# Performance work log

Measured on AMD Instinct MI355X. Metric: run time of the kernel, lower is better.

Reference implementation:

```python
import jax, jax.numpy as jnp
import numpy as np

N = 50000      # nodes
E = 800000     # edges (avg degree 16)
D_IN = 128
D_H = 128
D_OUT = 64
SLOPE = 0.2    # leaky-relu negative slope (from the 0.2 constants in the graph)


def setup_inputs() -> dict:
    key = jax.random.key(0)
    ks = jax.random.split(key, 18)
    def w(k, shape, fan_in):
        return jax.random.normal(k, shape, jnp.float32) / np.sqrt(fan_in)
    inp = {
        "x": jax.random.normal(ks[0], (N, D_IN), jnp.float32),
        "W0": w(ks[1], (D_IN, D_H), D_IN),
        "b0": jnp.zeros((D_H,), jnp.float32),
        "Wq1": w(ks[2], (D_H, D_H), D_H),
        "bq1": jnp.zeros((D_H,), jnp.float32),
        "Wp1": w(ks[3], (D_H, D_H), D_H),
        "bp1": jnp.zeros((D_H,), jnp.float32),
        "a1": 0.1 * w(ks[4], (D_H,), D_H),
        "bg2": jnp.zeros((D_H,), jnp.float32),
        "Wq2": w(ks[5], (D_H, D_OUT), D_H),
        "bq2": jnp.zeros((D_OUT,), jnp.float32),
        "Wp2": w(ks[6], (D_H, D_OUT), D_H),
        "bp2": jnp.zeros((D_OUT,), jnp.float32),
        "a2": 0.1 * w(ks[7], (D_OUT,), D_OUT),
        "b_out": jnp.zeros((D_OUT,), jnp.float32),
        "src": jax.random.randint(ks[8], (E,), 0, N),
        "dst": jax.random.randint(ks[9], (E,), 0, N),
        "num_nodes": N,
    }
    return inp


def _gat_block(m, src, dst, Wq, bq, Wp, bp, a, n):
    # m: [N, d_in]; q/p: [N, d]
    q = m @ Wq + bq
    p = m @ Wp + bp
    # edge scores: s_e = sum_d leaky_relu(q[dst_e] + p[src_e]) * a_d   [E]
    e = jax.nn.leaky_relu(q[dst] + p[src], SLOPE)          # [E, d]
    s = jnp.einsum("ed,d->e", e, a)                        # [E]
    es = jnp.exp(s)                                        # unstabilized exp, as in source graph
    denom = jax.ops.segment_sum(es, dst, num_segments=n)   # [N]
    alpha = es / denom[dst]                                # [E] edge softmax over incoming edges
    # aggregate messages alpha_e * p[src_e] into dst nodes
    agg = jax.ops.segment_sum(alpha[:, None] * p[src], dst, num_segments=n)  # [N, d]
    return agg


def reference(x, W0, b0, Wq1, bq1, Wp1, bp1, a1, bg2, Wq2, bq2, Wp2, bp2, a2, b_out, src, dst, num_nodes):
    m1 = jax.nn.gelu(x @ W0 + b0, approximate=False)       # erf GELU per graph constants
    h1 = _gat_block(m1, src, dst, Wq1, bq1, Wp1, bp1, a1, num_nodes)
    m2 = jax.nn.gelu(h1 + bg2, approximate=False)
    h2 = _gat_block(m2, src, dst, Wq2, bq2, Wp2, bp2, a2, num_nodes)
    return h2 + b_out
```

## Files before the change

kernel.cpp:

```cpp
#include <hip/hip_runtime.h>
#include <hip/hip_bf16.h>
#include <math.h>


#define SLOPE 0.2f

typedef __attribute__((ext_vector_type(8))) __bf16 bf16x8;
typedef __attribute__((ext_vector_type(4))) float f32x4;

__device__ __forceinline__ float gelu_erf(float x) {
    return 0.5f * x * (1.0f + erff(x * 0.70710678118654752f));
}

__device__ __forceinline__ unsigned short f2bf(float f) {
    unsigned int u = __float_as_uint(f);
    return (unsigned short)((u + 0x7fffu + ((u >> 16) & 1u)) >> 16);
}
__device__ __forceinline__ float bf2f(unsigned short h) {
    return __uint_as_float((unsigned int)h << 16);
}

__device__ __forceinline__ float row16_sum(float x) {
    x += __int_as_float(__builtin_amdgcn_update_dpp(0, __float_as_int(x), 0x121, 0xF, 0xF, true));
    x += __int_as_float(__builtin_amdgcn_update_dpp(0, __float_as_int(x), 0x122, 0xF, 0xF, true));
    x += __int_as_float(__builtin_amdgcn_update_dpp(0, __float_as_int(x), 0x124, 0xF, 0xF, true));
    x += __int_as_float(__builtin_amdgcn_update_dpp(0, __float_as_int(x), 0x128, 0xF, 0xF, true));
    return x;
}

__device__ __forceinline__ int swz(int off) { return off ^ ((off >> 4) & 0x70); }

__global__ __launch_bounds__(256) void pack_w(
    const float* __restrict__ W0,  const float* __restrict__ Wq1,
    const float* __restrict__ Wp1, const float* __restrict__ Wq2,
    const float* __restrict__ Wp2,
    unsigned short* __restrict__ P0,  unsigned short* __restrict__ Pq1,
    unsigned short* __restrict__ Pp1, unsigned short* __restrict__ Pq2,
    unsigned short* __restrict__ Pp2)
{
    const float* W; unsigned short* P; int C;
    switch (blockIdx.y) {
        case 0:  W = W0;  P = P0;  C = 128; break;
        case 1:  W = Wq1; P = Pq1; C = 128; break;
        case 2:  W = Wp1; P = Pp1; C = 128; break;
        case 3:  W = Wq2; P = Pq2; C = 64;  break;
        default: W = Wp2; P = Pp2; C = 64;  break;
    }
    int i = blockIdx.x * 256 + threadIdx.x;
    int CE = C * 128;
    if (i >= CE) return;
    int j = i & 7, l = (i >> 3) & 63, ks = (i >> 9) & 3, ct = i >> 11;
    int k = ks * 32 + ((l >> 4) << 3) + j;
    int n = ct * 16 + (l & 15);
    float v = W[k * C + n];
    unsigned short hb = f2bf(v);
    P[i] = hb;
    P[CE + i] = f2bf(v - bf2f(hb));
}

template <int C, bool TWO, int EPI>
__global__ __launch_bounds__(256) void mfma_gemm(
    const float* __restrict__ Af,
    const unsigned short* __restrict__ AHg, const unsigned short* __restrict__ ALg,
    const unsigned short* __restrict__ P1, const float* __restrict__ b1,
    const unsigned short* __restrict__ P2, const float* __restrict__ b2,
    float* __restrict__ outq, unsigned short* __restrict__ outp,
    unsigned short* __restrict__ o1hi, unsigned short* __restrict__ o1lo,
    int N)
{
    constexpr int CE  = C * 128;
    constexpr int CTT = (TWO ? 2 : 1) * (C / 16);
    constexpr int CTW = CTT / 4;
    constexpr int QCT = C / 16;

    __shared__ __align__(16) unsigned char lds[32768];

    const int t = threadIdx.x;
    const int lane = t & 63;
    const int w = t >> 6;
    const int row0 = blockIdx.x * 64;
    const int mcol = lane & 15;
    const int hk = lane >> 4;

    if constexpr (EPI == 0) {
#pragma unroll
        for (int i = 0; i < 8; i++) {
            int idx = t + i * 256;
            int row = idx >> 5;
            int gr = row0 + row;
            float4 v = make_float4(0.f, 0.f, 0.f, 0.f);
            if (gr < N) v = *reinterpret_cast<const float4*>(Af + (size_t)gr * 128 + (idx & 31) * 4);
            const float* f = reinterpret_cast<const float*>(&v);
            unsigned int h[4], l[4];
#pragma unroll
            for (int j = 0; j < 4; j++) {
                unsigned short hb = f2bf(f[j]);
                h[j] = hb;
                l[j] = f2bf(f[j] - bf2f(hb));
            }
            int so = swz(row * 256 + (idx & 31) * 8);
            *reinterpret_cast<uint2*>(&lds[so])         = make_uint2(h[0] | (h[1] << 16), h[2] | (h[3] << 16));
            *reinterpret_cast<uint2*>(&lds[16384 + so]) = make_uint2(l[0] | (l[1] << 16), l[2] | (l[3] << 16));
        }
    } else {
#pragma unroll
        for (int i = 0; i < 4; i++) {
            int idx = t + i * 256;
            int row = idx >> 4;
            int gr = row0 + row;
            uint4 vh = make_uint4(0, 0, 0, 0), vl = make_uint4(0, 0, 0, 0);
            if (gr < N) {
                vh = *reinterpret_cast<const uint4*>(AHg + (size_t)gr * 128 + (idx & 15) * 8);
                vl = *reinterpret_cast<const uint4*>(ALg + (size_t)gr * 128 + (idx & 15) * 8);
            }
            int so = swz(row * 256 + (idx & 15) * 16);
            *reinterpret_cast<uint4*>(&lds[so])         = vh;
            *reinterpret_cast<uint4*>(&lds[16384 + so]) = vl;
        }
    }
    __syncthreads();

    f32x4 acc[CTW][4];
#pragma unroll
    for (int c = 0; c < CTW; c++)
#pragma unroll
        for (int rf = 0; rf < 4; rf++) acc[c][rf] = (f32x4){0.f, 0.f, 0.f, 0.f};

#pragma unroll
    for (int ks = 0; ks < 4; ks++) {
        bf16x8 ah[4], al[4];
#pragma unroll
        for (int rf = 0; rf < 4; rf++) {
            int so = swz((rf * 16 + mcol) * 256 + ks * 64 + hk * 16);
            ah[rf] = *reinterpret_cast<const bf16x8*>(&lds[so]);
            al[rf] = *reinterpret_cast<const bf16x8*>(&lds[16384 + so]);
        }
#pragma unroll
        for (int c = 0; c < CTW; c++) {
            int ctg = w * CTW + c;
            bool isq = (!TWO) || (ctg < QCT);
            int ct = isq ? ctg : ctg - QCT;
            const unsigned short* P = isq ? P1 : P2;
            const unsigned short* Wp = P + ((ct * 4 + ks) * 64 + lane) * 8;
            bf16x8 bh = *reinterpret_cast<const bf16x8*>(Wp);
            bf16x8 bl = *reinterpret_cast<const bf16x8*>(Wp + CE);
#pragma unroll
            for (int rf = 0; rf < 4; rf++) {
                acc[c][rf] = __builtin_amdgcn_mfma_f32_16x16x32_bf16(ah[rf], bh, acc[c][rf], 0, 0, 0);
                acc[c][rf] = __builtin_amdgcn_mfma_f32_16x16x32_bf16(al[rf], bh, acc[c][rf], 0, 0, 0);
                acc[c][rf] = __builtin_amdgcn_mfma_f32_16x16x32_bf16(ah[rf], bl, acc[c][rf], 0, 0, 0);
            }
        }
    }

    __syncthreads();

    if constexpr (EPI == 0) {
#pragma unroll
        for (int c = 0; c < CTW; c++) {
            int col = (w * CTW + c) * 16 + mcol;
            float bv = b1[col];
#pragma unroll
            for (int rf = 0; rf < 4; rf++) {
#pragma unroll
                for (int r = 0; r < 4; r++) {
                    int row = rf * 16 + hk * 4 + r;
                    float v = gelu_erf(acc[c][rf][r] + bv);
                    unsigned short hb = f2bf(v);
                    int bo = row * 256 + col * 2;
                    *reinterpret_cast<unsigned short*>(&lds[swz(bo)])         = hb;
                    *reinterpret_cast<unsigned short*>(&lds[16384 + swz(bo)]) = f2bf(v - bf2f(hb));
                }
            }
        }
        __syncthreads();
#pragma unroll
        for (int i = 0; i < 8; i++) {
            int idx = t + i * 256;
            int pl = idx >> 10;
            int j = idx & 1023;
            int row = j >> 4;
            int gr = row0 + row;
            if (gr < N) {
                uint4 v = *reinterpret_cast<const uint4*>(&lds[pl * 16384 + swz(row * 256 + (j & 15) * 16)]);
                unsigned short* dp = pl ? o1lo : o1hi;
                *reinterpret_cast<uint4*>(dp + (size_t)gr * 128 + (j & 15) * 8) = v;
            }
        }
    } else {
#pragma unroll
        for (int c = 0; c < CTW; c++) {
            int ctg = w * CTW + c;
            bool isq = ctg < QCT;
            int ct = isq ? ctg : ctg - QCT;
            int col = ct * 16 + mcol;
            float bv = (isq ? b1 : b2)[col];
#pragma unroll
            for (int rf = 0; rf < 4; rf++) {
#pragma unroll
                for (int r = 0; r < 4; r++) {
                    int row = rf * 16 + hk * 4 + r;
                    int gr = row0 + row;
                    float v = acc[c][rf][r] + bv;
                    if (isq) {
                        if (gr < N) outq[(size_t)gr * C + col] = v;
                    } else {
                        *reinterpret_cast<unsigned short*>(&lds[swz(row * 256 + col * 2)]) = f2bf(v);
                    }
                }
            }
        }
        __syncthreads();
        constexpr int SLOTS = C / 8;
#pragma unroll
        for (int i = 0; i < (64 * SLOTS) / 256; i++) {
            int idx = t + i * 256;
            int row = idx / SLOTS;
            int sl = idx % SLOTS;
            int gr = row0 + row;
            if (gr < N)
                *reinterpret_cast<uint4*>(outp + (size_t)gr * C + sl * 8) =
                    *reinterpret_cast<const uint4*>(&lds[swz(row * 256 + sl * 16)]);
        }
    }
}


__global__ __launch_bounds__(256) void hist_coarse(
    const int* __restrict__ dst, int* __restrict__ gh, int E, int CB)
{
    __shared__ int cnt[4096];
    const int blk = blockIdx.x;
    const int t = threadIdx.x;
    for (int b = t; b < CB; b += 256) cnt[b] = 0;
    __syncthreads();
    const int epb = (E + 63) / 64;
    const int s = blk * epb;
    const int e_ = (s + epb < E) ? s + epb : E;
    for (int i = s + t; i < e_; i += 256)
        atomicAdd(&cnt[dst[i] >> 4], 1);
    __syncthreads();
    for (int b = t; b < CB; b += 256)
        gh[b * 64 + blk] = cnt[b];
}

__global__ __launch_bounds__(256) void scan1_kernel(const int* __restrict__ gh,
                                                    int* __restrict__ gscan,
                                                    int* __restrict__ bsum, int M)
{
    __shared__ int lds[256];
    int t = threadIdx.x;
    int i = blockIdx.x * 256 + t;
    int v = (i < M) ? gh[i] : 0;
    lds[t] = v;
    __syncthreads();
    int x = v;
    for (int off = 1; off < 256; off <<= 1) {
        int y = (t >= off) ? lds[t - off] : 0;
        __syncthreads();
        x += y;
        lds[t] = x;
        __syncthreads();
    }
    if (i < M) gscan[i] = x - v;
    if (t == 255) bsum[blockIdx.x] = x;
}

__global__ __launch_bounds__(1024) void scan2_kernel(int* __restrict__ bsum, int NB)
{
    __shared__ int lds[1024];
    int t = threadIdx.x;
    int v = (t < NB) ? bsum[t] : 0;
    lds[t] = v;
    __syncthreads();
    int x = v;
    for (int off = 1; off < 1024; off <<= 1) {
        int y = (t >= off) ? lds[t - off] : 0;
        __syncthreads();
        x += y;
        lds[t] = x;
        __syncthreads();
    }
    if (t < NB) bsum[t] = x - v;
}

__global__ __launch_bounds__(256) void scan3_kernel(int* __restrict__ gscan,
                                                    const int* __restrict__ bsum, int M)
{
    int i = blockIdx.x * 256 + threadIdx.x;
    if (i < M) gscan[i] += bsum[blockIdx.x];
}

__global__ __launch_bounds__(256) void scatter_coarse(
    const int* __restrict__ src, const int* __restrict__ dst,
    const int* __restrict__ gscan, int2* __restrict__ pairs, int E, int CB)
{
    __shared__ int cur[4096];
    const int blk = blockIdx.x;
    const int t = threadIdx.x;
    for (int b = t; b < CB; b += 256)
        cur[b] = gscan[b * 64 + blk];
    __syncthreads();
    const int epb = (E + 63) / 64;
    const int s = blk * epb;
    const int e_ = (s + epb < E) ? s + epb : E;
    for (int i = s + t; i < e_; i += 256) {
        int d = dst[i];
        int sv = src[i];
        int pos = atomicAdd(&cur[d >> 4], 1);
        pairs[pos] = make_int2(d, sv);
    }
}

__global__ __launch_bounds__(256) void finalize_kernel(
    const int2* __restrict__ pairs, const int* __restrict__ gscan,
    int* __restrict__ offs, int* __restrict__ csr_src, int N, int E, int CB)
{
    const int wid = blockIdx.x * 4 + (threadIdx.x >> 6);
    const int lane = threadIdx.x & 63;
    if (wid >= CB) return;

    const int s    = gscan[wid * 64];
    const int e_   = (wid + 1 < CB) ? gscan[(wid + 1) * 64] : E;
    const int base = wid * 16;
    const unsigned long long ltmask = (lane == 63) ? ~0ull >> 1
                                                   : (1ull << lane) - 1ull;

    int rc[16];
#pragma unroll
    for (int j = 0; j < 16; j++) rc[j] = 0;
    for (int c0 = s; c0 < e_; c0 += 64) {
        int i = c0 + lane;
        int d = (i < e_) ? pairs[i].x - base : -1;
#pragma unroll
        for (int j = 0; j < 16; j++)
            rc[j] += (int)__popcll(__ballot(d == j));
    }

    int pref[16];
    int run = s;
#pragma unroll
    for (int j = 0; j < 16; j++) { pref[j] = run; run += rc[j]; }
    int pref_v = 0;
#pragma unroll
    for (int j = 0; j < 16; j++) pref_v = (lane == j) ? pref[j] : pref_v;

    if (lane < 16 && base + lane < N) offs[base + lane] = pref_v;
    if (wid == CB - 1 && lane == 16) offs[N] = E;

    int rcv = 0;
    for (int c0 = s; c0 < e_; c0 += 64) {
        int i = c0 + lane;
        const bool act = i < e_;
        int2 pr = act ? pairs[i] : make_int2(base - 1, 0);
        int d = pr.x - base;
        unsigned long long msel = 0;
        int addcnt = 0;
#pragma unroll
        for (int j = 0; j < 16; j++) {
            unsigned long long m = __ballot(d == j);
            if (d == j) msel = m;
            if (lane == j) addcnt = (int)__popcll(m);
        }
        int subrank = (int)__popcll(msel & ltmask);
        int posbase = __builtin_amdgcn_ds_bpermute(d * 4, pref_v + rcv);
        if (act) csr_src[posbase + subrank] = pr.y;
        rcv += addcnt;
    }
}

template <int D, int EPI>
__global__ __launch_bounds__(256) void gat_agg(
    const float* __restrict__ q, const unsigned short* __restrict__ p,
    const float* __restrict__ a, const float* __restrict__ bvec,
    const int* __restrict__ offs, const int* __restrict__ csr_src,
    float* __restrict__ out, unsigned short* __restrict__ mhi,
    unsigned short* __restrict__ mlo, int N)
{
    constexpr int VPL = D / 16;
    const int t = threadIdx.x;
    const int lane = t & 63;
    const int sl = lane & 15;
    const int base = sl * VPL;
    const int node = blockIdx.x * 16 + ((t >> 6) << 2) + (lane >> 4);
    const bool valid = node < N;

    float qv[VPL], a6[VPL], a4[VPL], acc[VPL];
#pragma unroll
    for (int v = 0; v < VPL; v++) { qv[v] = 0.f; acc[v] = 0.f; }
    if (valid) {
        const float* qp = q + (size_t)node * D + base;
        float4 q0 = *reinterpret_cast<const float4*>(qp);
        qv[0] = q0.x; qv[1] = q0.y; qv[2] = q0.z; qv[3] = q0.w;
        if constexpr (VPL == 8) {
            float4 q1 = *reinterpret_cast<const float4*>(qp + 4);
            qv[4] = q1.x; qv[5] = q1.y; qv[6] = q1.z; qv[7] = q1.w;
        }
    }
#pragma unroll
    for (int v = 0; v < VPL; v++) {
        float av = a[base + v];
        a6[v] = 0.6f * av;
        a4[v] = 0.4f * av;
    }

    auto gather = [&](int s) -> uint4 {
        if constexpr (D == 128) {
            return *reinterpret_cast<const uint4*>(p + (size_t)s * 128 + base);
        } else {
            uint2 u = *reinterpret_cast<const uint2*>(p + (size_t)s * 64 + base);
            return make_uint4(u.x, u.y, 0u, 0u);
        }
    };
    auto unpack = [&](uint4 u, float* pv) {
        pv[0] = __uint_as_float(u.x << 16); pv[1] = __uint_as_float(u.x & 0xffff0000u);
        pv[2] = __uint_as_float(u.y << 16); pv[3] = __uint_as_float(u.y & 0xffff0000u);
        if constexpr (VPL == 8) {
            pv[4] = __uint_as_float(u.z << 16); pv[5] = __uint_as_float(u.z & 0xffff0000u);
            pv[6] = __uint_as_float(u.w << 16); pv[7] = __uint_as_float(u.w & 0xffff0000u);
        }
    };

    float denom = 0.f;
    int e  = valid ? offs[node] : 0;
    int e1 = valid ? offs[node + 1] : 0;

    int s0 = csr_src[(e + 0 < e1) ? e + 0 : 0];
    int s1 = csr_src[(e + 1 < e1) ? e + 1 : 0];
    int s2 = csr_src[(e + 2 < e1) ? e + 2 : 0];
    int s3 = csr_src[(e + 3 < e1) ? e + 3 : 0];
    uint4 uA0 = gather(s0), uA1 = gather(s1), uA2 = gather(s2), uA3 = gather(s3);
    int en = e + 4;
    int n0 = csr_src[(en + 0 < e1) ? en + 0 : 0];
    int n1 = csr_src[(en + 1 < e1) ? en + 1 : 0];
    int n2 = csr_src[(en + 2 < e1) ? en + 2 : 0];
    int n3 = csr_src[(en + 3 < e1) ? en + 3 : 0];

    while (__any(e < e1)) {
        const bool a0 = (e + 0) < e1, a1b = (e + 1) < e1,
                   a2 = (e + 2) < e1, a3 = (e + 3) < e1;

        uint4 v0 = gather(n0), v1 = gather(n1), v2 = gather(n2), v3 = gather(n3);

        const int em = en + 4;
        const int m0 = csr_src[(em + 0 < e1) ? em + 0 : 0];
        const int m1 = csr_src[(em + 1 < e1) ? em + 1 : 0];
        const int m2 = csr_src[(em + 2 < e1) ? em + 2 : 0];
        const int m3 = csr_src[(em + 3 < e1) ? em + 3 : 0];

        float pv[4][VPL];
        unpack(uA0, pv[0]); unpack(uA1, pv[1]); unpack(uA2, pv[2]); unpack(uA3, pv[3]);

        float pa0 = 0.f, pa1 = 0.f, pa2 = 0.f, pa3 = 0.f;
#pragma unroll
        for (int v = 0; v < VPL; v++) {
            float d0 = qv[v] + pv[0][v];
            float d1 = qv[v] + pv[1][v];
            float d2 = qv[v] + pv[2][v];
            float d3 = qv[v] + pv[3][v];
            pa0 = fmaf(d0, a6[v], pa0); pa0 = fmaf(fabsf(d0), a4[v], pa0);
            pa1 = fmaf(d1, a6[v], pa1); pa1 = fmaf(fabsf(d1), a4[v], pa1);
            pa2 = fmaf(d2, a6[v], pa2); pa2 = fmaf(fabsf(d2), a4[v], pa2);
            pa3 = fmaf(d3, a6[v], pa3); pa3 = fmaf(fabsf(d3), a4[v], pa3);
        }

        float r0 = row16_sum(pa0);
        float r1 = row16_sum(pa1);
        float r2 = row16_sum(pa2);
        float r3 = row16_sum(pa3);

        float esm0 = a0  ? __expf(r0) : 0.f;
        float esm1 = a1b ? __expf(r1) : 0.f;
        float esm2 = a2  ? __expf(r2) : 0.f;
        float esm3 = a3  ? __expf(r3) : 0.f;
        denom += (esm0 + esm1) + (esm2 + esm3);
#pragma unroll
        for (int v = 0; v < VPL; v++) {
            acc[v] = fmaf(esm0, pv[0][v], acc[v]);
            acc[v] = fmaf(esm1, pv[1][v], acc[v]);
            acc[v] = fmaf(esm2, pv[2][v], acc[v]);
            acc[v] = fmaf(esm3, pv[3][v], acc[v]);
        }

        uA0 = v0; uA1 = v1; uA2 = v2; uA3 = v3;
        n0 = m0; n1 = m1; n2 = m2; n3 = m3;
        e = en; en = em;
    }

    if (!valid) return;
    float inv = (denom != 0.f) ? 1.f / denom : 0.f;
    if constexpr (EPI == 0) {
        union { unsigned short us[8]; uint4 v; } H, L;
#pragma unroll
        for (int v = 0; v < VPL; v++) {
            float g = gelu_erf(acc[v] * inv + bvec[base + v]);
            H.us[v] = f2bf(g);
            L.us[v] = f2bf(g - bf2f(H.us[v]));
        }
        *reinterpret_cast<uint4*>(mhi + (size_t)node * 128 + base) = H.v;
        *reinterpret_cast<uint4*>(mlo + (size_t)node * 128 + base) = L.v;
    } else {
        union { float f[4]; float4 v; } O;
#pragma unroll
        for (int v = 0; v < VPL; v++) O.f[v] = acc[v] * inv + bvec[base + v];
        *reinterpret_cast<float4*>(out + (size_t)node * D + base) = O.v;
    }
}

extern "C" void kernel_launch(void* const* d_in, const int* in_sizes, int n_in,
                              void* d_out, int out_size, void* d_ws, size_t ws_size,
                              hipStream_t stream)
{
    const float* x     = (const float*)d_in[0];
    const float* W0    = (const float*)d_in[1];
    const float* b0    = (const float*)d_in[2];
    const float* Wq1   = (const float*)d_in[3];
    const float* bq1   = (const float*)d_in[4];
    const float* Wp1   = (const float*)d_in[5];
    const float* bp1   = (const float*)d_in[6];
    const float* a1    = (const float*)d_in[7];
    const float* bg2   = (const float*)d_in[8];
    const float* Wq2   = (const float*)d_in[9];
    const float* bq2   = (const float*)d_in[10];
    const float* Wp2   = (const float*)d_in[11];
    const float* bp2   = (const float*)d_in[12];
    const float* a2    = (const float*)d_in[13];
    const float* b_out = (const float*)d_in[14];
    const int*   src   = (const int*)d_in[15];
    const int*   dst   = (const int*)d_in[16];

    const int N = in_sizes[0] / 128;
    const int E = in_sizes[15];
    float* out = (float*)d_out;

    float* q_buf        = (float*)d_ws;
    unsigned short* pb  = (unsigned short*)(q_buf + (size_t)N * 128);
    unsigned short* Mhi = pb + (size_t)N * 128;
    unsigned short* Mlo = Mhi + (size_t)N * 128;
    unsigned short* P0  = Mlo + (size_t)N * 128;
    unsigned short* Pq1 = P0  + 128 * 128 * 2;
    unsigned short* Pp1 = Pq1 + 128 * 128 * 2;
    unsigned short* Pq2 = Pp1 + 128 * 128 * 2;
    unsigned short* Pp2 = Pq2 + 128 * 64 * 2;
    int* offs    = (int*)(Pp2 + 128 * 64 * 2);
    int* csr_src = offs + (N + 2);
    const int CB = (N + 15) / 16;
    const int M  = CB * 64;
    int* gh    = csr_src + E;
    int* gscan = gh + M;
    int* bsum  = gscan + M;
    int2* pairs = (int2*)q_buf;

    const int NB1 = (M + 255) / 256;

    pack_w<<<dim3(64, 5), 256, 0, stream>>>(W0, Wq1, Wp1, Wq2, Wp2,
                                            P0, Pq1, Pp1, Pq2, Pp2);
    hist_coarse<<<64, 256, 0, stream>>>(dst, gh, E, CB);
    scan1_kernel<<<NB1, 256, 0, stream>>>(gh, gscan, bsum, M);
    scan2_kernel<<<1, 1024, 0, stream>>>(bsum, NB1);
    scan3_kernel<<<NB1, 256, 0, stream>>>(gscan, bsum, M);
    scatter_coarse<<<64, 256, 0, stream>>>(src, dst, gscan, pairs, E, CB);
    finalize_kernel<<<(CB + 3) / 4, 256, 0, stream>>>(pairs, gscan, offs, csr_src, N, E, CB);

    const int GB64 = (N + 63) / 64;
    const int GGAT = (N + 15) / 16;

    mfma_gemm<128, false, 0><<<GB64, 256, 0, stream>>>(
        x, nullptr, nullptr, P0, b0, nullptr, nullptr,
        nullptr, nullptr, Mhi, Mlo, N);
    mfma_gemm<128, true, 1><<<GB64, 256, 0, stream>>>(
        nullptr, Mhi, Mlo, Pq1, bq1, Pp1, bp1,
        q_buf, pb, nullptr, nullptr, N);
    gat_agg<128, 0><<<GGAT, 256, 0, stream>>>(
        q_buf, pb, a1, bg2, offs, csr_src,
        nullptr, Mhi, Mlo, N);
    mfma_gemm<64, true, 1><<<GB64, 256, 0, stream>>>(
        nullptr, Mhi, Mlo, Pq2, bq2, Pp2, bp2,
        q_buf, pb, nullptr, nullptr, N);
    gat_agg<64, 1><<<GGAT, 256, 0, stream>>>(
        q_buf, pb, a2, b_out, offs, csr_src,
        out, nullptr, nullptr, N);
}
```

Before: 283.6 us.

## Fuse input GEMM with layer-1 q/p projection GEMM via LDS

Merges the first GEMM (x@W0 + GELU) and the layer-1 q/p projection GEMM into one kernel. The GELU output stays in LDS as a bf16 hi/lo split and is fed directly into the second GEMM, so the Mhi/Mlo intermediates are no longer written to and read back from global memory, and one launch goes away. The template GEMM is also specialised into a separate 64-column kernel for layer 2. The cost is a heavier kernel with more accumulator registers, which may reduce occupancy.

```diff
diff --git a/kernel.cpp b/kernel.cpp
--- a/kernel.cpp
+++ b/kernel.cpp
@@ -58,21 +58,14 @@
     P[CE + i] = f2bf(v - bf2f(hb));
 }
 
-template <int C, bool TWO, int EPI>
-__global__ __launch_bounds__(256) void mfma_gemm(
-    const float* __restrict__ Af,
-    const unsigned short* __restrict__ AHg, const unsigned short* __restrict__ ALg,
-    const unsigned short* __restrict__ P1, const float* __restrict__ b1,
-    const unsigned short* __restrict__ P2, const float* __restrict__ b2,
-    float* __restrict__ outq, unsigned short* __restrict__ outp,
-    unsigned short* __restrict__ o1hi, unsigned short* __restrict__ o1lo,
-    int N)
-{
-    constexpr int CE  = C * 128;
-    constexpr int CTT = (TWO ? 2 : 1) * (C / 16);
-    constexpr int CTW = CTT / 4;
-    constexpr int QCT = C / 16;
-
+__global__ __launch_bounds__(256) void gemm_fused01(
+    const float* __restrict__ x,
+    const unsigned short* __restrict__ P0,  const float* __restrict__ b0,
+    const unsigned short* __restrict__ Pq1, const float* __restrict__ bq1,
+    const unsigned short* __restrict__ Pp1, const float* __restrict__ bp1,
+    float* __restrict__ outq, unsigned short* __restrict__ outp, int N)
+{
+    constexpr int CE = 128 * 128;
     __shared__ __align__(16) unsigned char lds[32768];
 
     const int t = threadIdx.x;
@@ -82,49 +75,32 @@
     const int mcol = lane & 15;
     const int hk = lane >> 4;
 
-    if constexpr (EPI == 0) {
-#pragma unroll
-        for (int i = 0; i < 8; i++) {
-            int idx = t + i * 256;
-            int row = idx >> 5;
-            int gr = row0 + row;
-            float4 v = make_float4(0.f, 0.f, 0.f, 0.f);
-            if (gr < N) v = *reinterpret_cast<const float4*>(Af + (size_t)gr * 128 + (idx & 31) * 4);
-            const float* f = reinterpret_cast<const float*>(&v);
-            unsigned int h[4], l[4];
-#pragma unroll
-            for (int j = 0; j < 4; j++) {
-                unsigned short hb = f2bf(f[j]);
-                h[j] = hb;
-                l[j] = f2bf(f[j] - bf2f(hb));
-            }
-            int so = swz(row * 256 + (idx & 31) * 8);
-            *reinterpret_cast<uint2*>(&lds[so])         = make_uint2(h[0] | (h[1] << 16), h[2] | (h[3] << 16));
-            *reinterpret_cast<uint2*>(&lds[16384 + so]) = make_uint2(l[0] | (l[1] << 16), l[2] | (l[3] << 16));
-        }
-    } else {
-#pragma unroll
-        for (int i = 0; i < 4; i++) {
-            int idx = t + i * 256;
-            int row = idx >> 4;
-            int gr = row0 + row;
-            uint4 vh = make_uint4(0, 0, 0, 0), vl = make_uint4(0, 0, 0, 0);
-            if (gr < N) {
-                vh = *reinterpret_cast<const uint4*>(AHg + (size_t)gr * 128 + (idx & 15) * 8);
-                vl = *reinterpret_cast<const uint4*>(ALg + (size_t)gr * 128 + (idx & 15) * 8);
-            }
-            int so = swz(row * 256 + (idx & 15) * 16);
-            *reinterpret_cast<uint4*>(&lds[so])         = vh;
-            *reinterpret_cast<uint4*>(&lds[16384 + so]) = vl;
-        }
-    }
-    __syncthreads();
-
-    f32x4 acc[CTW][4];
-#pragma unroll
-    for (int c = 0; c < CTW; c++)
-#pragma unroll
-        for (int rf = 0; rf < 4; rf++) acc[c][rf] = (f32x4){0.f, 0.f, 0.f, 0.f};
+#pragma unroll
+    for (int i = 0; i < 8; i++) {
+        int idx = t + i * 256;
+        int row = idx >> 5;
+        int gr = row0 + row;
+        float4 v = make_float4(0.f, 0.f, 0.f, 0.f);
+        if (gr < N) v = *reinterpret_cast<const float4*>(x + (size_t)gr * 128 + (idx & 31) * 4);
+        const float* f = reinterpret_cast<const float*>(&v);
+        unsigned int h[4], l[4];
+#pragma unroll
+        for (int j = 0; j < 4; j++) {
+            unsigned short hb = f2bf(f[j]);
+            h[j] = hb;
+            l[j] = f2bf(f[j] - bf2f(hb));
+        }
+        int so = swz(row * 256 + (idx & 31) * 8);
+        *reinterpret_cast<uint2*>(&lds[so])         = make_uint2(h[0] | (h[1] << 16), h[2] | (h[3] << 16));
+        *reinterpret_cast<uint2*>(&lds[16384 + so]) = make_uint2(l[0] | (l[1] << 16), l[2] | (l[3] << 16));
+    }
+    __syncthreads();
+
+    f32x4 acc1[2][4];
+#pragma unroll
+    for (int c = 0; c < 2; c++)
+#pragma unroll
+        for (int rf = 0; rf < 4; rf++) acc1[c][rf] = (f32x4){0.f, 0.f, 0.f, 0.f};
 
 #pragma unroll
     for (int ks = 0; ks < 4; ks++) {
@@ -136,12 +112,161 @@
             al[rf] = *reinterpret_cast<const bf16x8*>(&lds[16384 + so]);
         }
 #pragma unroll
-        for (int c = 0; c < CTW; c++) {
-            int ctg = w * CTW + c;
-            bool isq = (!TWO) || (ctg < QCT);
-            int ct = isq ? ctg : ctg - QCT;
-            const unsigned short* P = isq ? P1 : P2;
-            const unsigned short* Wp = P + ((ct * 4 + ks) * 64 + lane) * 8;
+        for (int c = 0; c < 2; c++) {
+            int ct = w * 2 + c;
+            const unsigned short* Wp = P0 + ((ct * 4 + ks) * 64 + lane) * 8;
+            bf16x8 bh = *reinterpret_cast<const bf16x8*>(Wp);
+            bf16x8 bl = *reinterpret_cast<const bf16x8*>(Wp + CE);
+#pragma unroll
+            for (int rf = 0; rf < 4; rf++) {
+                acc1[c][rf] = __builtin_amdgcn_mfma_f32_16x16x32_bf16(ah[rf], bh, acc1[c][rf], 0, 0, 0);
+                acc1[c][rf] = __builtin_amdgcn_mfma_f32_16x16x32_bf16(al[rf], bh, acc1[c][rf], 0, 0, 0);
+                acc1[c][rf] = __builtin_amdgcn_mfma_f32_16x16x32_bf16(ah[rf], bl, acc1[c][rf], 0, 0, 0);
+            }
+        }
+    }
+    __syncthreads();
+
+#pragma unroll
+    for (int c = 0; c < 2; c++) {
+        int col = (w * 2 + c) * 16 + mcol;
+        float bv = b0[col];
+#pragma unroll
+        for (int rf = 0; rf < 4; rf++) {
+#pragma unroll
+            for (int r = 0; r < 4; r++) {
+                int row = rf * 16 + hk * 4 + r;
+                float v = gelu_erf(acc1[c][rf][r] + bv);
+                unsigned short hb = f2bf(v);
+                int bo = row * 256 + col * 2;
+                *reinterpret_cast<unsigned short*>(&lds[swz(bo)])         = hb;
+                *reinterpret_cast<unsigned short*>(&lds[16384 + swz(bo)]) = f2bf(v - bf2f(hb));
+            }
+        }
+    }
+    __syncthreads();
+
+    f32x4 acc2[4][4];
+#pragma unroll
+    for (int c = 0; c < 4; c++)
+#pragma unroll
+        for (int rf = 0; rf < 4; rf++) acc2[c][rf] = (f32x4){0.f, 0.f, 0.f, 0.f};
+
+#pragma unroll
+    for (int ks = 0; ks < 4; ks++) {
+        bf16x8 ah[4], al[4];
+#pragma unroll
+        for (int rf = 0; rf < 4; rf++) {
+            int so = swz((rf * 16 + mcol) * 256 + ks * 64 + hk * 16);
+            ah[rf] = *reinterpret_cast<const bf16x8*>(&lds[so]);
+            al[rf] = *reinterpret_cast<const bf16x8*>(&lds[16384 + so]);
+        }
+#pragma unroll
+        for (int c = 0; c < 4; c++) {
+            int ctg = w * 4 + c;
+            bool isq = ctg < 8;
+            int ct = isq ? ctg : ctg - 8;
+            const unsigned short* Wp = (isq ? Pq1 : Pp1) + ((ct * 4 + ks) * 64 + lane) * 8;
+            bf16x8 bh = *reinterpret_cast<const bf16x8*>(Wp);
+            bf16x8 bl = *reinterpret_cast<const bf16x8*>(Wp + CE);
+#pragma unroll
+            for (int rf = 0; rf < 4; rf++) {
+                acc2[c][rf] = __builtin_amdgcn_mfma_f32_16x16x32_bf16(ah[rf], bh, acc2[c][rf], 0, 0, 0);
+                acc2[c][rf] = __builtin_amdgcn_mfma_f32_16x16x32_bf16(al[rf], bh, acc2[c][rf], 0, 0, 0);
+                acc2[c][rf] = __builtin_amdgcn_mfma_f32_16x16x32_bf16(ah[rf], bl, acc2[c][rf], 0, 0, 0);
+            }
+        }
+    }
+    __syncthreads();
+
+#pragma unroll
+    for (int c = 0; c < 4; c++) {
+        int ctg = w * 4 + c;
+        bool isq = ctg < 8;
+        int ct = isq ? ctg : ctg - 8;
+        int col = ct * 16 + mcol;
+        float bv = (isq ? bq1 : bp1)[col];
+#pragma unroll
+        for (int rf = 0; rf < 4; rf++) {
+#pragma unroll
+            for (int r = 0; r < 4; r++) {
+                int row = rf * 16 + hk * 4 + r;
+                int gr = row0 + row;
+                float v = acc2[c][rf][r] + bv;
+                if (isq) {
+                    if (gr < N) outq[(size_t)gr * 128 + col] = v;
+                } else {
+                    *reinterpret_cast<unsigned short*>(&lds[swz(row * 256 + col * 2)]) = f2bf(v);
+                }
+            }
+        }
+    }
+    __syncthreads();
+#pragma unroll
+    for (int i = 0; i < 4; i++) {
+        int idx = t + i * 256;
+        int row = idx >> 4;
+        int sl = idx & 15;
+        int gr = row0 + row;
+        if (gr < N)
+            *reinterpret_cast<uint4*>(outp + (size_t)gr * 128 + sl * 8) =
+                *reinterpret_cast<const uint4*>(&lds[swz(row * 256 + sl * 16)]);
+    }
+}
+
+__global__ __launch_bounds__(256) void mfma_gemm64(
+    const unsigned short* __restrict__ AHg, const unsigned short* __restrict__ ALg,
+    const unsigned short* __restrict__ P1, const float* __restrict__ b1,
+    const unsigned short* __restrict__ P2, const float* __restrict__ b2,
+    float* __restrict__ outq, unsigned short* __restrict__ outp, int N)
+{
+    constexpr int CE = 64 * 128;
+    __shared__ __align__(16) unsigned char lds[32768];
+
+    const int t = threadIdx.x;
+    const int lane = t & 63;
+    const int w = t >> 6;
+    const int row0 = blockIdx.x * 64;
+    const int mcol = lane & 15;
+    const int hk = lane >> 4;
+
+#pragma unroll
+    for (int i = 0; i < 4; i++) {
+        int idx = t + i * 256;
+        int row = idx >> 4;
+        int gr = row0 + row;
+        uint4 vh = make_uint4(0, 0, 0, 0), vl = make_uint4(0, 0, 0, 0);
+        if (gr < N) {
+            vh = *reinterpret_cast<const uint4*>(AHg + (size_t)gr * 128 + (idx & 15) * 8);
+            vl = *reinterpret_cast<const uint4*>(ALg + (size_t)gr * 128 + (idx & 15) * 8);
+        }
+        int so = swz(row * 256 + (idx & 15) * 16);
+        *reinterpret_cast<uint4*>(&lds[so])         = vh;
+        *reinterpret_cast<uint4*>(&lds[16384 + so]) = vl;
+    }
+    __syncthreads();
+
+    f32x4 acc[2][4];
+#pragma unroll
+    for (int c = 0; c < 2; c++)
+#pragma unroll
+        for (int rf = 0; rf < 4; rf++) acc[c][rf] = (f32x4){0.f, 0.f, 0.f, 0.f};
+
+#pragma unroll
+    for (int ks = 0; ks < 4; ks++) {
+        bf16x8 ah[4], al[4];
+#pragma unroll
+        for (int rf = 0; rf < 4; rf++) {
+            int so = swz((rf * 16 + mcol) * 256 + ks * 64 + hk * 16);
+            ah[rf] = *reinterpret_cast<const bf16x8*>(&lds[so]);
+            al[rf] = *reinterpret_cast<const bf16x8*>(&lds[16384 + so]);
+        }
+#pragma unroll
+        for (int c = 0; c < 2; c++) {
+            int ctg = w * 2 + c;
+            bool isq = ctg < 4;
+            int ct = isq ? ctg : ctg - 4;
+            const unsigned short* Wp = (isq ? P1 : P2) + ((ct * 4 + ks) * 64 + lane) * 8;
             bf16x8 bh = *reinterpret_cast<const bf16x8*>(Wp);
             bf16x8 bl = *reinterpret_cast<const bf16x8*>(Wp + CE);
 #pragma unroll
@@ -152,76 +277,40 @@
             }
         }
     }
-
-    __syncthreads();
-
-    if constexpr (EPI == 0) {
-#pragma unroll
-        for (int c = 0; c < CTW; c++) {
-            int col = (w * CTW + c) * 16 + mcol;
-            float bv = b1[col];
-#pragma unroll
-            for (int rf = 0; rf < 4; rf++) {
-#pragma unroll
-                for (int r = 0; r < 4; r++) {
-                    int row = rf * 16 + hk * 4 + r;
-                    float v = gelu_erf(acc[c][rf][r] + bv);
-                    unsigned short hb = f2bf(v);
-                    int bo = row * 256 + col * 2;
-                    *reinterpret_cast<unsigned short*>(&lds[swz(bo)])         = hb;
-                    *reinterpret_cast<unsigned short*>(&lds[16384 + swz(bo)]) = f2bf(v - bf2f(hb));
+    __syncthreads();
+
+#pragma unroll
+    for (int c = 0; c < 2; c++) {
+        int ctg = w * 2 + c;
+        bool isq = ctg < 4;
+        int ct = isq ? ctg : ctg - 4;
+        int col = ct * 16 + mcol;
+        float bv = (isq ? b1 : b2)[col];
+#pragma unroll
+        for (int rf = 0; rf < 4; rf++) {
+#pragma unroll
+            for (int r = 0; r < 4; r++) {
+                int row = rf * 16 + hk * 4 + r;
+                int gr = row0 + row;
+                float v = acc[c][rf][r] + bv;
+                if (isq) {
+                    if (gr < N) outq[(size_t)gr * 64 + col] = v;
+                } else {
+                    *reinterpret_cast<unsigned short*>(&lds[swz(row * 256 + col * 2)]) = f2bf(v);
                 }
             }
         }
-        __syncthreads();
-#pragma unroll
-        for (int i = 0; i < 8; i++) {
-            int idx = t + i * 256;
-            int pl = idx >> 10;
-            int j = idx & 1023;
-            int row = j >> 4;
-            int gr = row0 + row;
-            if (gr < N) {
-                uint4 v = *reinterpret_cast<const uint4*>(&lds[pl * 16384 + swz(row * 256 + (j & 15) * 16)]);
-                unsigned short* dp = pl ? o1lo : o1hi;
-                *reinterpret_cast<uint4*>(dp + (size_t)gr * 128 + (j & 15) * 8) = v;
-            }
-        }
-    } else {
-#pragma unroll
-        for (int c = 0; c < CTW; c++) {
-            int ctg = w * CTW + c;
-            bool isq = ctg < QCT;
-            int ct = isq ? ctg : ctg - QCT;
-            int col = ct * 16 + mcol;
-            float bv = (isq ? b1 : b2)[col];
-#pragma unroll
-            for (int rf = 0; rf < 4; rf++) {
-#pragma unroll
-                for (int r = 0; r < 4; r++) {
-                    int row = rf * 16 + hk * 4 + r;
-                    int gr = row0 + row;
-                    float v = acc[c][rf][r] + bv;
-                    if (isq) {
-                        if (gr < N) outq[(size_t)gr * C + col] = v;
-                    } else {
-                        *reinterpret_cast<unsigned short*>(&lds[swz(row * 256 + col * 2)]) = f2bf(v);
-                    }
-                }
-            }
-        }
-        __syncthreads();
-        constexpr int SLOTS = C / 8;
-#pragma unroll
-        for (int i = 0; i < (64 * SLOTS) / 256; i++) {
-            int idx = t + i * 256;
-            int row = idx / SLOTS;
-            int sl = idx % SLOTS;
-            int gr = row0 + row;
-            if (gr < N)
-                *reinterpret_cast<uint4*>(outp + (size_t)gr * C + sl * 8) =
-                    *reinterpret_cast<const uint4*>(&lds[swz(row * 256 + sl * 16)]);
-        }
+    }
+    __syncthreads();
+#pragma unroll
+    for (int i = 0; i < 2; i++) {
+        int idx = t + i * 256;
+        int row = idx >> 3;
+        int sl = idx & 7;
+        int gr = row0 + row;
+        if (gr < N)
+            *reinterpret_cast<uint4*>(outp + (size_t)gr * 64 + sl * 8) =
+                *reinterpret_cast<const uint4*>(&lds[swz(row * 256 + sl * 16)]);
     }
 }
 
@@ -565,18 +654,14 @@
     const int GB64 = (N + 63) / 64;
     const int GGAT = (N + 15) / 16;
 
-    mfma_gemm<128, false, 0><<<GB64, 256, 0, stream>>>(
-        x, nullptr, nullptr, P0, b0, nullptr, nullptr,
-        nullptr, nullptr, Mhi, Mlo, N);
-    mfma_gemm<128, true, 1><<<GB64, 256, 0, stream>>>(
-        nullptr, Mhi, Mlo, Pq1, bq1, Pp1, bp1,
-        q_buf, pb, nullptr, nullptr, N);
+    gemm_fused01<<<GB64, 256, 0, stream>>>(
+        x, P0, b0, Pq1, bq1, Pp1, bp1, q_buf, pb, N);
     gat_agg<128, 0><<<GGAT, 256, 0, stream>>>(
         q_buf, pb, a1, bg2, offs, csr_src,
         nullptr, Mhi, Mlo, N);
-    mfma_gemm<64, true, 1><<<GB64, 256, 0, stream>>>(
-        nullptr, Mhi, Mlo, Pq2, bq2, Pp2, bp2,
-        q_buf, pb, nullptr, nullptr, N);
+    mfma_gemm64<<<GB64, 256, 0, stream>>>(
+        Mhi, Mlo, Pq2, bq2, Pp2, bp2,
+        q_buf, pb, N);
     gat_agg<64, 1><<<GGAT, 256, 0, stream>>>(
         q_buf, pb, a2, b_out, offs, csr_src,
         out, nullptr, nullptr, N);
```

Measured after the change: 279.4 us. No clear change (-1.5%).
